# Kernel tuning notes

Hardware: AMD Instinct MI355X
Metric: run time of the kernel (lower is better)

## Reference

```python
import jax, jax.numpy as jnp
import numpy as np

B, S, H, E = 32, 2048, 1024, 1024
NEG = -10000000000.0


def setup_inputs() -> dict:
    key = jax.random.key(0)
    ks = jax.random.split(key, 8)
    scale = 1.0 / np.sqrt(H)
    return {
        "hidden": jax.random.normal(ks[0], (B, H), jnp.float32),
        "encoder_outputs": jax.random.normal(ks[1], (B, S, E), jnp.float32),
        "mask": jax.random.randint(ks[2], (B, S), 0, 2, jnp.int32),
        "W_h": jax.random.normal(ks[3], (H, H), jnp.float32) * scale,
        "b_h": jax.random.normal(ks[4], (H,), jnp.float32) * scale,
        "W_e": jax.random.normal(ks[5], (E, H), jnp.float32) * scale,
        "b_e": jax.random.normal(ks[6], (H,), jnp.float32) * scale,
        "v": jax.random.normal(ks[7], (H,), jnp.float32) * scale,
    }


def reference(hidden, encoder_outputs, mask, W_h, b_h, W_e, b_e, v):
    # hidden proj: (B,H) -> (B,1,H); encoder proj: (B,S,E) -> (B,S,H)
    h_proj = (hidden @ W_h + b_h)[:, None, :]
    e_proj = jnp.einsum("bse,eh->bsh", encoder_outputs, W_e) + b_e
    energy = jnp.tanh(h_proj + e_proj)                      # (B,S,H)
    attention = jnp.einsum("bsh,h->bs", energy, v)          # (B,S)
    attention = jnp.where(mask == 0, NEG, attention)
    attention_weights = jax.nn.softmax(attention, axis=1)   # (B,S)
    context = jnp.einsum("bs,bse->be", attention_weights, encoder_outputs)
    return (context, attention_weights)
```

## Files before the change

kernel.cpp:

```cpp
#include <hip/hip_runtime.h>

#define NEGV -10000000000.0f

typedef _Float16 half8 __attribute__((ext_vector_type(8)));
typedef float f32x4 __attribute__((ext_vector_type(4)));

__device__ __forceinline__ void gld16(const void* g, void* l) {
  __builtin_amdgcn_global_load_lds((const __attribute__((address_space(1))) void*)g,
                                   (__attribute__((address_space(3))) void*)l,
                                   16, 0, 0);
}

__device__ __forceinline__ float fast_tanh(float x) {
  const float e = __expf(2.0f * x);
  return 1.0f - 2.0f * __builtin_amdgcn_rcpf(e + 1.0f);
}

__global__ void encconv_kernel(const float* __restrict__ enc, _Float16* __restrict__ enc16) {
  const size_t base = ((size_t)blockIdx.x * 256 + threadIdx.x) * 8;
  const float4 x = *(const float4*)(enc + base);
  const float4 y = *(const float4*)(enc + base + 4);
  half8 h;
  h[0] = (_Float16)x.x; h[1] = (_Float16)x.y; h[2] = (_Float16)x.z; h[3] = (_Float16)x.w;
  h[4] = (_Float16)y.x; h[5] = (_Float16)y.y; h[6] = (_Float16)y.z; h[7] = (_Float16)y.w;
  *(half8*)(enc16 + base) = h;
}

__global__ void wconv_kernel(const float* __restrict__ We, _Float16* __restrict__ W16T) {
  __shared__ float tile[32][33];
  const int tx = threadIdx.x, ty = threadIdx.y;
  const int n0 = blockIdx.x * 32, k0 = blockIdx.y * 32;
  tile[ty][tx] = We[(size_t)(k0 + ty) * 1024 + n0 + tx];
  __syncthreads();
  W16T[(size_t)(n0 + ty) * 1024 + k0 + tx] = (_Float16)tile[tx][ty];
}

__global__ void hproj_kernel(const float* __restrict__ hidden, const float* __restrict__ W_h,
                             const float* __restrict__ b_h, const float* __restrict__ b_e,
                             float* __restrict__ hpb) {
  const int b = blockIdx.x >> 2;
  const int h = ((blockIdx.x & 3) << 8) | threadIdx.x;
  const float* hb = hidden + b * 1024;
  float a0 = 0.f, a1 = 0.f, a2 = 0.f, a3 = 0.f;
  #pragma unroll 4
  for (int k = 0; k < 1024; k += 4) {
    a0 = fmaf(hb[k + 0], W_h[(size_t)(k + 0) * 1024 + h], a0);
    a1 = fmaf(hb[k + 1], W_h[(size_t)(k + 1) * 1024 + h], a1);
    a2 = fmaf(hb[k + 2], W_h[(size_t)(k + 2) * 1024 + h], a2);
    a3 = fmaf(hb[k + 3], W_h[(size_t)(k + 3) * 1024 + h], a3);
  }
  hpb[b * 1024 + h] = b_h[h] + b_e[h] + ((a0 + a1) + (a2 + a3));
}

__global__ __launch_bounds__(512, 2) void attn_gemm8_kernel(
    const _Float16* __restrict__ enc16, const _Float16* __restrict__ W16T,
    const float* __restrict__ hpb, const float* __restrict__ v,
    const int* __restrict__ mask, float* __restrict__ logits) {
  __shared__ __align__(16) _Float16 Abuf[3][256 * 32];
  __shared__ __align__(16) _Float16 Bbuf[3][256 * 32];
  __shared__ float hp_s[1024];
  __shared__ float vh_s[1024];
  __shared__ float red[256 * 4];

  const int tid = threadIdx.x;
  const int wid = tid >> 6;
  const int lane = tid & 63;
  const int l15 = lane & 15;
  const int qq = lane >> 4;
  const int wr = wid >> 2;
  const int wc = wid & 3;
  const int m0 = blockIdx.x << 8;
  const int b = blockIdx.x >> 3;

  for (int i = tid; i < 1024; i += 512) {
    hp_s[i] = hpb[(b << 10) + i];
    vh_s[i] = v[i];
  }

  const char* encb = (const char*)(enc16 + (size_t)m0 * 1024);
  const char* wbase = (const char*)W16T;

  auto stageA = [&](int buf, int t) {
    const int kb = (t & 31) << 6;
    char* db = (char*)(&Abuf[buf][0]) + (wid << 10);
    #pragma unroll
    for (int i = 0; i < 2; ++i) {
      const int gd = tid + (i << 9);
      const int row = gd >> 2;
      const int g = gd & 3;
      const int col = kb + ((g ^ ((row >> 2) & 3)) << 4);
      gld16(encb + (size_t)row * 2048 + col, db + (i << 13));
    }
  };
  auto stageB = [&](int buf, int t) {
    const int kb = (t & 31) << 6;
    const char* wb = wbase + (size_t)(t >> 5) * 256 * 2048;
    char* db = (char*)(&Bbuf[buf][0]) + (wid << 10);
    #pragma unroll
    for (int i = 0; i < 2; ++i) {
      const int gd = tid + (i << 9);
      const int np = gd >> 2;
      const int g = gd & 3;
      const int col = kb + ((g ^ ((np >> 2) & 3)) << 4);
      gld16(wb + (size_t)np * 2048 + col, db + (i << 13));
    }
  };

  f32x4 acc[8][4];
  float rowsum[8][4];
  #pragma unroll
  for (int mi = 0; mi < 8; ++mi)
    #pragma unroll
    for (int j = 0; j < 4; ++j) {
      acc[mi][j] = (f32x4){0.f, 0.f, 0.f, 0.f};
      rowsum[mi][j] = 0.f;
    }

  stageA(0, 0); stageB(0, 0);
  stageA(1, 1); stageB(1, 1);
  __syncthreads();

  const int swz = (qq ^ (l15 >> 2)) << 4;
  int bi = 0;
  #pragma unroll 1
  for (int t = 0; t < 128; ++t) {
    const int bi2 = (bi >= 1) ? bi - 1 : bi + 2;
    const char* A = (const char*)(&Abuf[bi][0]);
    const char* B = (const char*)(&Bbuf[bi][0]);
    half8 a[4], bf[4];

    #pragma unroll
    for (int mi = 0; mi < 4; ++mi) {
      const int row = (wr << 7) + (mi << 4) + l15;
      a[mi] = *(const half8*)(A + (row << 6) + swz);
    }
    #pragma unroll
    for (int ni = 0; ni < 4; ++ni) {
      const int np = (wc << 6) + (ni << 4) + l15;
      bf[ni] = *(const half8*)(B + (np << 6) + swz);
    }
    if (t < 126) stageA(bi2, t + 2);
    __builtin_amdgcn_s_barrier();
    asm volatile("s_waitcnt lgkmcnt(0)" ::: "memory");
    __builtin_amdgcn_s_setprio(1);
    #pragma unroll
    for (int mi = 0; mi < 4; ++mi)
      #pragma unroll
      for (int ni = 0; ni < 4; ++ni)
        acc[mi][ni] = __builtin_amdgcn_mfma_f32_16x16x32_f16(a[mi], bf[ni], acc[mi][ni], 0, 0, 0);
    __builtin_amdgcn_s_setprio(0);
    __builtin_amdgcn_s_barrier();

    #pragma unroll
    for (int mi = 0; mi < 4; ++mi) {
      const int row = (wr << 7) + 64 + (mi << 4) + l15;
      a[mi] = *(const half8*)(A + (row << 6) + swz);
    }
    if (t < 126) stageB(bi2, t + 2);
    __builtin_amdgcn_s_barrier();
    asm volatile("s_waitcnt lgkmcnt(0)" ::: "memory");
    __builtin_amdgcn_s_setprio(1);
    #pragma unroll
    for (int mi = 0; mi < 4; ++mi)
      #pragma unroll
      for (int ni = 0; ni < 4; ++ni)
        acc[4 + mi][ni] = __builtin_amdgcn_mfma_f32_16x16x32_f16(a[mi], bf[ni], acc[4 + mi][ni], 0, 0, 0);
    __builtin_amdgcn_s_setprio(0);

    if (t < 126) asm volatile("s_waitcnt vmcnt(4)" ::: "memory");
    else         asm volatile("s_waitcnt vmcnt(0)" ::: "memory");
    __builtin_amdgcn_s_barrier();

    if ((t & 31) == 31) {
      const int nt = t >> 5;
      const int hb = (nt << 8) + (wc << 6);
      #pragma unroll
      for (int ni = 0; ni < 4; ++ni) {
        const int h = hb + (ni << 4) + l15;
        const float hv = hp_s[h];
        const float vv = vh_s[h];
        #pragma unroll
        for (int mi = 0; mi < 8; ++mi) {
          #pragma unroll
          for (int r = 0; r < 4; ++r)
            rowsum[mi][r] += fast_tanh(acc[mi][ni][r] + hv) * vv;
          acc[mi][ni] = (f32x4){0.f, 0.f, 0.f, 0.f};
        }
      }
    }
    bi = (bi >= 2) ? 0 : bi + 1;
  }

  #pragma unroll
  for (int mi = 0; mi < 8; ++mi)
    #pragma unroll
    for (int r = 0; r < 4; ++r) {
      float s = rowsum[mi][r];
      s += __shfl_xor(s, 1);
      s += __shfl_xor(s, 2);
      s += __shfl_xor(s, 4);
      s += __shfl_xor(s, 8);
      rowsum[mi][r] = s;
    }
  __syncthreads();
  if (l15 == 0) {
    #pragma unroll
    for (int mi = 0; mi < 8; ++mi)
      #pragma unroll
      for (int r = 0; r < 4; ++r) {
        const int row = (wr << 7) + (mi << 4) + (qq << 2) + r;
        red[(row << 2) + wc] = rowsum[mi][r];
      }
  }
  __syncthreads();
  if (tid < 256) {
    const float s = red[tid << 2] + red[(tid << 2) + 1] + red[(tid << 2) + 2] + red[(tid << 2) + 3];
    const int m = m0 + tid;
    logits[m] = (mask[(b << 11) + (m & 2047)] == 0) ? NEGV : s;
  }
}

__global__ void softmax_kernel(const float* __restrict__ logits, float* __restrict__ wout) {
  __shared__ float red[4];
  const int b = blockIdx.x, tid = threadIdx.x;
  const int wid = tid >> 6, lane = tid & 63;
  const float* lb = logits + b * 2048;
  float x[8];
  #pragma unroll
  for (int j = 0; j < 8; ++j) x[j] = lb[tid + j * 256];
  float m = x[0];
  #pragma unroll
  for (int j = 1; j < 8; ++j) m = fmaxf(m, x[j]);
  #pragma unroll
  for (int off = 32; off > 0; off >>= 1) m = fmaxf(m, __shfl_xor(m, off));
  if (lane == 0) red[wid] = m;
  __syncthreads();
  m = fmaxf(fmaxf(red[0], red[1]), fmaxf(red[2], red[3]));
  __syncthreads();
  float e[8];
  float s = 0.f;
  #pragma unroll
  for (int j = 0; j < 8; ++j) { e[j] = expf(x[j] - m); s += e[j]; }
  #pragma unroll
  for (int off = 32; off > 0; off >>= 1) s += __shfl_xor(s, off);
  if (lane == 0) red[wid] = s;
  __syncthreads();
  s = red[0] + red[1] + red[2] + red[3];
  const float inv = 1.0f / s;
  #pragma unroll
  for (int j = 0; j < 8; ++j) wout[b * 2048 + tid + j * 256] = e[j] * inv;
}

__global__ void context16_kernel(const _Float16* __restrict__ enc16,
                                 const float* __restrict__ wout, float* __restrict__ ctx) {
  const int b = blockIdx.x >> 4;
  const int ch = blockIdx.x & 15;
  const int tl = threadIdx.x & 127;
  const int sh = threadIdx.x >> 7;
  float a[8] = {0.f, 0.f, 0.f, 0.f, 0.f, 0.f, 0.f, 0.f};
  #pragma unroll 1
  for (int i = 0; i < 64; ++i) {
    const int s = (ch << 7) + (i << 1) + sh;
    const float w = wout[(b << 11) + s];
    const half8 r = *(const half8*)(enc16 + (((size_t)(b << 11) + s) << 10) + (tl << 3));
    #pragma unroll
    for (int j = 0; j < 8; ++j) a[j] = fmaf(w, (float)r[j], a[j]);
  }
  float* c = ctx + (b << 10) + (tl << 3);
  #pragma unroll
  for (int j = 0; j < 8; ++j) atomicAdd(c + j, a[j]);
}

extern "C" void kernel_launch(void* const* d_in, const int* in_sizes, int n_in,
                              void* d_out, int out_size, void* d_ws, size_t ws_size,
                              hipStream_t stream) {
  const float* hidden = (const float*)d_in[0];
  const float* enc    = (const float*)d_in[1];
  const int*   mask   = (const int*)d_in[2];
  const float* W_h    = (const float*)d_in[3];
  const float* b_h    = (const float*)d_in[4];
  const float* W_e    = (const float*)d_in[5];
  const float* b_e    = (const float*)d_in[6];
  const float* v      = (const float*)d_in[7];

  float* ctx  = (float*)d_out;
  float* wout = (float*)d_out + 32 * 1024;

  char* ws = (char*)d_ws;
  const size_t ENC16_BYTES = 134217728ULL;
  _Float16* enc16 = (_Float16*)ws;
  _Float16* W16T  = (_Float16*)(ws + ENC16_BYTES);
  float* hpb      = (float*)(ws + ENC16_BYTES + 2097152);
  float* logits   = (float*)(ws + ENC16_BYTES + 2097152 + 131072);

  hipMemsetAsync(ctx, 0, 32 * 1024 * sizeof(float), stream);
  hipLaunchKernelGGL(encconv_kernel, dim3(32768), dim3(256), 0, stream, enc, enc16);
  hipLaunchKernelGGL(wconv_kernel, dim3(32, 32), dim3(32, 32), 0, stream, W_e, W16T);
  hipLaunchKernelGGL(hproj_kernel, dim3(128), dim3(256), 0, stream, hidden, W_h, b_h, b_e, hpb);
  hipLaunchKernelGGL(attn_gemm8_kernel, dim3(256), dim3(512), 0, stream,
                     enc16, W16T, hpb, v, mask, logits);
  hipLaunchKernelGGL(softmax_kernel, dim3(32), dim3(256), 0, stream, logits, wout);
  hipLaunchKernelGGL(context16_kernel, dim3(512), dim3(256), 0, stream, enc16, wout, ctx);
}
```

Baseline: 311.1 us.

## Restructure GEMM pipeline to double-buffered 128-wide K steps with split halves

Replaces the triple-buffered 64-element K-tile loop with a two-parity double buffer where each iteration covers 128 K elements split into two half-tiles. This halves the loop trip count and barrier overhead per K element, and staging of the next tile is spread across four MFMA phases. It also changes the LDS swizzle to use (row>>1)&3 and precomputes per-lane LDS offsets to save address arithmetic. LDS use rises from three to four buffers per operand, and the hand-tuned vmcnt waits must exactly match the issue order, so any miscount risks a race.

```diff
diff --git a/kernel.cpp b/kernel.cpp
--- a/kernel.cpp
+++ b/kernel.cpp
@@ -56,11 +56,11 @@
     const _Float16* __restrict__ enc16, const _Float16* __restrict__ W16T,
     const float* __restrict__ hpb, const float* __restrict__ v,
     const int* __restrict__ mask, float* __restrict__ logits) {
-  __shared__ __align__(16) _Float16 Abuf[3][256 * 32];
-  __shared__ __align__(16) _Float16 Bbuf[3][256 * 32];
+  __shared__ __align__(16) _Float16 Abuf[2][2][256 * 32];
+  __shared__ __align__(16) _Float16 Bbuf[2][2][256 * 32];
   __shared__ float hp_s[1024];
   __shared__ float vh_s[1024];
-  __shared__ float red[256 * 4];
+  __shared__ float red[1024];
 
   const int tid = threadIdx.x;
   const int wid = tid >> 6;
@@ -77,34 +77,43 @@
     vh_s[i] = v[i];
   }
 
+  const int r0 = tid >> 2;
+  const int r1 = r0 + 128;
+  const int g0 = tid & 3;
+  const int sc = (g0 ^ ((r0 >> 1) & 3)) << 4;
+  const int ldsoff0 = (wid << 10);
+  const int ldsoff1 = (wid << 10) + 8192;
+
   const char* encb = (const char*)(enc16 + (size_t)m0 * 1024);
-  const char* wbase = (const char*)W16T;
-
-  auto stageA = [&](int buf, int t) {
-    const int kb = (t & 31) << 6;
-    char* db = (char*)(&Abuf[buf][0]) + (wid << 10);
-    #pragma unroll
-    for (int i = 0; i < 2; ++i) {
-      const int gd = tid + (i << 9);
-      const int row = gd >> 2;
-      const int g = gd & 3;
-      const int col = kb + ((g ^ ((row >> 2) & 3)) << 4);
-      gld16(encb + (size_t)row * 2048 + col, db + (i << 13));
+  const char* wb0 = (const char*)W16T;
+
+  auto stageA = [&](int par, int kh, int t) {
+    const int colb = ((t & 15) << 7) + (kh << 6) + sc;
+    char* base = (char*)(&Abuf[par][kh][0]);
+    gld16(encb + (size_t)r0 * 2048 + colb, base + ldsoff0);
+    gld16(encb + (size_t)r1 * 2048 + colb, base + ldsoff1);
+  };
+  auto stageB = [&](int par, int kh, int t) {
+    const char* wb = wb0 + ((size_t)(t >> 4) << 19);
+    const int colb = ((t & 15) << 7) + (kh << 6) + sc;
+    char* base = (char*)(&Bbuf[par][kh][0]);
+    gld16(wb + (size_t)r0 * 2048 + colb, base + ldsoff0);
+    gld16(wb + (size_t)r1 * 2048 + colb, base + ldsoff1);
+  };
+
+  int aoff[2][4], boff[4];
+  #pragma unroll
+  for (int mh = 0; mh < 2; ++mh)
+    #pragma unroll
+    for (int mi = 0; mi < 4; ++mi) {
+      const int row = (wr << 7) + (mh << 6) + (mi << 4) + l15;
+      aoff[mh][mi] = (row << 6) + ((qq ^ ((row >> 1) & 3)) << 4);
     }
-  };
-  auto stageB = [&](int buf, int t) {
-    const int kb = (t & 31) << 6;
-    const char* wb = wbase + (size_t)(t >> 5) * 256 * 2048;
-    char* db = (char*)(&Bbuf[buf][0]) + (wid << 10);
-    #pragma unroll
-    for (int i = 0; i < 2; ++i) {
-      const int gd = tid + (i << 9);
-      const int np = gd >> 2;
-      const int g = gd & 3;
-      const int col = kb + ((g ^ ((np >> 2) & 3)) << 4);
-      gld16(wb + (size_t)np * 2048 + col, db + (i << 13));
-    }
-  };
+  #pragma unroll
+  for (int ni = 0; ni < 4; ++ni) {
+    const int np = (wc << 6) + (ni << 4) + l15;
+    boff[ni] = (np << 6) + ((qq ^ ((np >> 1) & 3)) << 4);
+  }
 
   f32x4 acc[8][4];
   float rowsum[8][4];
@@ -116,30 +125,26 @@
       rowsum[mi][j] = 0.f;
     }
 
-  stageA(0, 0); stageB(0, 0);
-  stageA(1, 1); stageB(1, 1);
-  __syncthreads();
-
-  const int swz = (qq ^ (l15 >> 2)) << 4;
-  int bi = 0;
+  stageA(0, 0, 0); stageB(0, 0, 0);
+  stageA(0, 1, 0); stageB(0, 1, 0);
+  asm volatile("s_waitcnt vmcnt(4) lgkmcnt(0)" ::: "memory");
+  __builtin_amdgcn_s_barrier();
+
   #pragma unroll 1
-  for (int t = 0; t < 128; ++t) {
-    const int bi2 = (bi >= 1) ? bi - 1 : bi + 2;
-    const char* A = (const char*)(&Abuf[bi][0]);
-    const char* B = (const char*)(&Bbuf[bi][0]);
+  for (int t = 0; t < 64; ++t) {
+    const int par = t & 1, npar = par ^ 1;
+    const char* A0 = (const char*)(&Abuf[par][0][0]);
+    const char* A1 = (const char*)(&Abuf[par][1][0]);
+    const char* B0 = (const char*)(&Bbuf[par][0][0]);
+    const char* B1 = (const char*)(&Bbuf[par][1][0]);
+    const bool more = t < 63;
     half8 a[4], bf[4];
 
     #pragma unroll
-    for (int mi = 0; mi < 4; ++mi) {
-      const int row = (wr << 7) + (mi << 4) + l15;
-      a[mi] = *(const half8*)(A + (row << 6) + swz);
-    }
-    #pragma unroll
-    for (int ni = 0; ni < 4; ++ni) {
-      const int np = (wc << 6) + (ni << 4) + l15;
-      bf[ni] = *(const half8*)(B + (np << 6) + swz);
-    }
-    if (t < 126) stageA(bi2, t + 2);
+    for (int mi = 0; mi < 4; ++mi) a[mi] = *(const half8*)(A0 + aoff[0][mi]);
+    #pragma unroll
+    for (int ni = 0; ni < 4; ++ni) bf[ni] = *(const half8*)(B0 + boff[ni]);
+    if (more) { stageA(npar, 0, t + 1); stageB(npar, 0, t + 1); }
     __builtin_amdgcn_s_barrier();
     asm volatile("s_waitcnt lgkmcnt(0)" ::: "memory");
     __builtin_amdgcn_s_setprio(1);
@@ -152,11 +157,8 @@
     __builtin_amdgcn_s_barrier();
 
     #pragma unroll
-    for (int mi = 0; mi < 4; ++mi) {
-      const int row = (wr << 7) + 64 + (mi << 4) + l15;
-      a[mi] = *(const half8*)(A + (row << 6) + swz);
-    }
-    if (t < 126) stageB(bi2, t + 2);
+    for (int mi = 0; mi < 4; ++mi) a[mi] = *(const half8*)(A0 + aoff[1][mi]);
+    if (more) stageA(npar, 1, t + 1);
     __builtin_amdgcn_s_barrier();
     asm volatile("s_waitcnt lgkmcnt(0)" ::: "memory");
     __builtin_amdgcn_s_setprio(1);
@@ -166,13 +168,42 @@
       for (int ni = 0; ni < 4; ++ni)
         acc[4 + mi][ni] = __builtin_amdgcn_mfma_f32_16x16x32_f16(a[mi], bf[ni], acc[4 + mi][ni], 0, 0, 0);
     __builtin_amdgcn_s_setprio(0);
-
-    if (t < 126) asm volatile("s_waitcnt vmcnt(4)" ::: "memory");
-    else         asm volatile("s_waitcnt vmcnt(0)" ::: "memory");
-    __builtin_amdgcn_s_barrier();
-
-    if ((t & 31) == 31) {
-      const int nt = t >> 5;
+    if (more) asm volatile("s_waitcnt vmcnt(6)" ::: "memory");
+    else      asm volatile("s_waitcnt vmcnt(0)" ::: "memory");
+    __builtin_amdgcn_s_barrier();
+
+    #pragma unroll
+    for (int mi = 0; mi < 4; ++mi) a[mi] = *(const half8*)(A1 + aoff[0][mi]);
+    #pragma unroll
+    for (int ni = 0; ni < 4; ++ni) bf[ni] = *(const half8*)(B1 + boff[ni]);
+    if (more) stageB(npar, 1, t + 1);
+    __builtin_amdgcn_s_barrier();
+    asm volatile("s_waitcnt lgkmcnt(0)" ::: "memory");
+    __builtin_amdgcn_s_setprio(1);
+    #pragma unroll
+    for (int mi = 0; mi < 4; ++mi)
+      #pragma unroll
+      for (int ni = 0; ni < 4; ++ni)
+        acc[mi][ni] = __builtin_amdgcn_mfma_f32_16x16x32_f16(a[mi], bf[ni], acc[mi][ni], 0, 0, 0);
+    __builtin_amdgcn_s_setprio(0);
+    __builtin_amdgcn_s_barrier();
+
+    #pragma unroll
+    for (int mi = 0; mi < 4; ++mi) a[mi] = *(const half8*)(A1 + aoff[1][mi]);
+    __builtin_amdgcn_s_barrier();
+    asm volatile("s_waitcnt lgkmcnt(0)" ::: "memory");
+    __builtin_amdgcn_s_setprio(1);
+    #pragma unroll
+    for (int mi = 0; mi < 4; ++mi)
+      #pragma unroll
+      for (int ni = 0; ni < 4; ++ni)
+        acc[4 + mi][ni] = __builtin_amdgcn_mfma_f32_16x16x32_f16(a[mi], bf[ni], acc[4 + mi][ni], 0, 0, 0);
+    __builtin_amdgcn_s_setprio(0);
+    asm volatile("s_waitcnt vmcnt(4)" ::: "memory");
+    __builtin_amdgcn_s_barrier();
+
+    if ((t & 15) == 15) {
+      const int nt = t >> 4;
       const int hb = (nt << 8) + (wc << 6);
       #pragma unroll
       for (int ni = 0; ni < 4; ++ni) {
@@ -188,7 +219,6 @@
         }
       }
     }
-    bi = (bi >= 2) ? 0 : bi + 1;
   }
 
   #pragma unroll
```

Result: slower. 325.0 us (+4.5%).
